# Kernel optimization log

Measured on AMD Instinct MI355X. Metric: run time of the kernel, lower is better.

Reference implementation:

```python
import jax, jax.numpy as jnp
import numpy as np

B, C, H, W = 16, 256, 32, 32
DIM = H * W  # LayerNorm/Linear dim == h*w per the rearrange in forward


def _conv1x1(x, w, b):
    # x: [b,c,h,w], w: [out,in] (1x1 kernel squeezed), b: [out]
    return jnp.einsum('bchw,oc->bohw', x, w) + b[None, :, None, None]


def _layernorm(x, g, b, eps=1e-5):
    mu = jnp.mean(x, axis=-1, keepdims=True)
    var = jnp.var(x, axis=-1, keepdims=True)
    return (x - mu) / jnp.sqrt(var + eps) * g + b


def setup_inputs() -> dict:
    key = jax.random.key(0)
    ks = jax.random.split(key, 12)
    n = jax.random.normal
    k_cdc = (2.0 / (2 * C)) ** 0.5   # kaiming_normal fan_in = 2C
    k_v = (2.0 / C) ** 0.5           # fan_in = C
    k_lin = (2.0 / DIM) ** 0.5       # fan_in = DIM
    return {
        'x_spa': n(ks[0], (B, C, H, W), jnp.float32),
        'x_freq': n(ks[1], (B, C, H, W), jnp.float32),
        'w_cdc': n(ks[2], (C, 2 * C), jnp.float32) * k_cdc,
        'b_cdc': jnp.zeros((C,), jnp.float32),
        'w_sv': n(ks[3], (C, C), jnp.float32) * k_v,
        'b_sv': jnp.zeros((C,), jnp.float32),
        'w_fv': n(ks[4], (C, C), jnp.float32) * k_v,
        'b_fv': jnp.zeros((C,), jnp.float32),
        'ln_w': jnp.ones((DIM,), jnp.float32),
        'ln_b': jnp.zeros((DIM,), jnp.float32),
        'w_qk': n(ks[5], (2 * DIM, DIM), jnp.float32) * k_lin,  # Linear(dim, 2*dim), no bias
        'w_spa': n(ks[6], (DIM, DIM), jnp.float32) * k_lin,
        'b_spa': jnp.zeros((DIM,), jnp.float32),
        'w_frq': n(ks[7], (DIM, DIM), jnp.float32) * k_lin,
        'b_frq': jnp.zeros((DIM,), jnp.float32),
    }


def reference(x_spa, x_freq, w_cdc, b_cdc, w_sv, b_sv, w_fv, b_fv,
              ln_w, ln_b, w_qk, w_spa, b_spa, w_frq, b_frq):
    b, c, h, w = x_spa.shape
    hw = h * w
    scale = hw ** (-0.5)
    v_spa = _conv1x1(x_spa, w_sv, b_sv).reshape(b, c, hw)
    v_freq = _conv1x1(x_freq, w_fv, b_fv).reshape(b, c, hw)
    x = _conv1x1(jnp.concatenate([x_spa, x_freq], axis=1), w_cdc, b_cdc).reshape(b, c, hw)
    x = _layernorm(x, ln_w, ln_b)
    qk = x @ w_qk.T                       # [b, c, 2*hw]
    q, k = jnp.split(qk, 2, axis=-1)      # each [b, c, hw]
    att = jnp.einsum('bcn,bcm->bnm', q, k) * scale   # q^T k over channels: [b, hw, hw]
    att_spa = jax.nn.softmax(att @ w_spa.T + b_spa, axis=-1)
    att_frq = jax.nn.softmax(att @ w_frq.T + b_frq, axis=-1)
    out_spa = x_spa + jnp.einsum('bcn,bnm->bcm', v_spa, att_spa).reshape(b, c, h, w)
    out_freq = x_freq + jnp.einsum('bcn,bnm->bcm', v_freq, att_frq).reshape(b, c, h, w)
    return out_spa, out_freq
```

## Files before the change

kernel.cpp:

```cpp
#include <hip/hip_runtime.h>
#include <hip/hip_bf16.h>

typedef __hip_bfloat16 bf16;
typedef __attribute__((ext_vector_type(8))) short bf16x8v;
typedef __attribute__((ext_vector_type(4))) float f32x4v;

__device__ __forceinline__ float bfbits2f(unsigned short h) {
    union { unsigned int u; float f; } v; v.u = ((unsigned int)h) << 16; return v.f;
}
__device__ __forceinline__ unsigned short f2bfbits(float f) {
    bf16 h = __float2bfloat16(f);
    unsigned short s;
    __builtin_memcpy(&s, &h, 2);
    return s;
}
__device__ __forceinline__ float load1_any(const void* p, long idx, bool f32) {
    if (f32) return ((const float*)p)[idx];
    return bfbits2f(((const unsigned short*)p)[idx]);
}
__device__ __forceinline__ float4 loadbf4(const bf16* p) {
    ushort4 u = *reinterpret_cast<const ushort4*>(p);
    return make_float4(bfbits2f(u.x), bfbits2f(u.y), bfbits2f(u.z), bfbits2f(u.w));
}
__device__ __forceinline__ void store_bf4(bf16* p, float a, float b, float c, float d) {
    ushort4 o;
    o.x = f2bfbits(a); o.y = f2bfbits(b); o.z = f2bfbits(c); o.w = f2bfbits(d);
    *reinterpret_cast<ushort4*>(p) = o;
}
__device__ __forceinline__ void gl16(const void* g, void* l) {
    __builtin_amdgcn_global_load_lds(
        (const __attribute__((address_space(1))) unsigned int*)g,
        (__attribute__((address_space(3))) unsigned int*)l, 16, 0, 0);
}

__global__ __launch_bounds__(1024)
void detect_kernel(const unsigned short* __restrict__ x, int* __restrict__ flag) {
    const int tid = threadIdx.x;
    int zc = 0, hc = 0;
    const uint4* xv = (const uint4*)x;
#pragma unroll
    for (int p = 0; p < 16; ++p) {
        uint4 v = xv[p * 1024 + tid];
        unsigned s0 = v.x & 0xFFFFu, s1 = v.y & 0xFFFFu;
        unsigned s2 = v.z & 0xFFFFu, s3 = v.w & 0xFFFFu;
        zc += (int)(s0 == 0) + (int)(s1 == 0) + (int)(s2 == 0) + (int)(s3 == 0);
        hc += (int)(((s0 >> 7) & 0xFFu) >= 0x90u) + (int)(((s1 >> 7) & 0xFFu) >= 0x90u)
            + (int)(((s2 >> 7) & 0xFFu) >= 0x90u) + (int)(((s3 >> 7) & 0xFFu) >= 0x90u);
    }
#pragma unroll
    for (int off = 32; off > 0; off >>= 1) {
        zc += __shfl_down(zc, off);
        hc += __shfl_down(hc, off);
    }
    __shared__ int rz[16], rh[16];
    if ((tid & 63) == 0) { rz[tid >> 6] = zc; rh[tid >> 6] = hc; }
    __syncthreads();
    if (tid == 0) {
        int Z = 0, H = 0;
#pragma unroll
        for (int i = 0; i < 16; ++i) { Z += rz[i]; H += rh[i]; }
        flag[0] = (Z > 60000 || H > 256) ? 1 : 0;
        flag[1] = 1;
    }
}

__global__ void diag_kernel(float* __restrict__ out, float val) {
    if (threadIdx.x == 0) out[0] = val;
}

__global__ __launch_bounds__(256)
void convert6_kernel(const void* __restrict__ s0, const void* __restrict__ s1,
                     const void* __restrict__ s2, const void* __restrict__ s3,
                     const void* __restrict__ s4, const void* __restrict__ s5,
                     const void* __restrict__ b0, const void* __restrict__ b1,
                     const void* __restrict__ b2,
                     bf16* __restrict__ dst, bf16* __restrict__ wl,
                     float* __restrict__ bc, const int* __restrict__ dflag) {
    const bool f32 = (*dflag != 0);
    for (long i = (long)blockIdx.x * 256 + threadIdx.x; i < 4850432;
         i += (long)gridDim.x * 256) {
        if (i < 4456448) {
            const void* s; long o;
            if (i < 131072)       { s = s0; o = i; }
            else if (i < 196608)  { s = s1; o = i - 131072; }
            else if (i < 262144)  { s = s2; o = i - 196608; }
            else if (i < 2359296) { s = s3; o = i - 262144; }
            else if (i < 3407872) { s = s4; o = i - 2359296; }
            else                  { s = s5; o = i - 3407872; }
            dst[i] = __float2bfloat16(load1_any(s, o, f32));
        } else if (i < 4849664) {
            long j = i - 4456448;
            int r = (int)(j >> 9), c = (int)(j & 511);
            float v = 0.f;
            if (r < 256) v = load1_any(s0, r * 512 + c, f32);
            else if (r < 512) { if (c < 256) v = load1_any(s1, (r - 256) * 256 + c, f32); }
            else              { if (c >= 256) v = load1_any(s2, (r - 512) * 256 + (c - 256), f32); }
            wl[j] = __float2bfloat16(v);
        } else {
            long j = i - 4849664;
            float v = (j < 256) ? load1_any(b0, j, f32)
                    : (j < 512) ? load1_any(b1, j - 256, f32)
                                : load1_any(b2, j - 512, f32);
            bc[j] = v;
        }
    }
}

__global__ __launch_bounds__(256)
void xpose_w_kernel(const bf16* __restrict__ src, bf16* __restrict__ dst) {
    __shared__ float t[64][65];
    const int c0 = blockIdx.x * 64, r0 = blockIdx.y * 64;
    const int tid = threadIdx.x;
#pragma unroll
    for (int p = 0; p < 16; ++p) {
        int e = tid + p * 256; int r = e >> 6, c = e & 63;
        t[r][c] = __bfloat162float(src[(long)(r0 + r) * 1024 + c0 + c]);
    }
    __syncthreads();
#pragma unroll
    for (int p = 0; p < 16; ++p) {
        int e = tid + p * 256; int r = e >> 6, c = e & 63;
        dst[(long)(c0 + r) * 1024 + r0 + c] = __float2bfloat16(t[c][r]);
    }
}

__global__ __launch_bounds__(256)
void xpose_conv_kernel(const void* __restrict__ x1, const void* __restrict__ x2,
                       bf16* __restrict__ dst, int bofs, int zsplit,
                       const int* __restrict__ dflag) {
    const bool f32 = (*dflag != 0);
    __shared__ float t[64][65];
    const int ch0 = blockIdx.y * 64, n0 = blockIdx.x * 64, z = blockIdx.z;
    const bool hiz = (z >= zsplit);
    const int zl = hiz ? z - zsplit : z;
    const void* x = hiz ? x2 : x1;
    const long sb = (long)(zl + bofs) * 262144, db = (long)z * 262144;
    const int tid = threadIdx.x;
#pragma unroll
    for (int p = 0; p < 16; ++p) {
        int e = tid + p * 256; int sch = e >> 6, sn = e & 63;
        t[sch][sn] = load1_any(x, sb + (long)(ch0 + sch) * 1024 + n0 + sn, f32);
    }
    __syncthreads();
#pragma unroll
    for (int p = 0; p < 16; ++p) {
        int e = tid + p * 256; int dn = e >> 6, dch = e & 63;
        dst[db + (long)(n0 + dn) * 256 + ch0 + dch] = __float2bfloat16(t[dch][dn]);
    }
}

__global__ __launch_bounds__(256)
void smnorm_kernel(bf16* __restrict__ X, bf16* __restrict__ vb, int gN, int gq) {
    const int tid = threadIdx.x;
    const int cg = tid & 7;
    const int js = tid >> 3;
    const int n0 = blockIdx.x * 64;
    const long zb = (long)blockIdx.y * 1048576;
    unsigned short* Xp = (unsigned short*)X + zb + n0 + cg * 8;

    float m[8];
#pragma unroll
    for (int q = 0; q < 8; ++q) m[q] = -3.4e38f;
#pragma unroll 4
    for (int r = 0; r < 32; ++r) {
        bf16x8v u = *(const bf16x8v*)(Xp + (long)(js * 32 + r) * 1024);
#pragma unroll
        for (int q = 0; q < 8; ++q)
            m[q] = fmaxf(m[q], bfbits2f((unsigned short)u[q]));
    }
    __shared__ float sh[32][8][8];
    __shared__ float Mc[64];
    __shared__ float Sc[64];
#pragma unroll
    for (int q = 0; q < 8; ++q) sh[js][cg][q] = m[q];
    __syncthreads();
    if (tid < 64) {
        float mm = -3.4e38f;
#pragma unroll 8
        for (int s = 0; s < 32; ++s) mm = fmaxf(mm, sh[s][tid >> 3][tid & 7]);
        Mc[tid] = mm;
    }
    __syncthreads();
    float M8[8], s8[8];
#pragma unroll
    for (int q = 0; q < 8; ++q) { M8[q] = Mc[cg * 8 + q]; s8[q] = 0.f; }
#pragma unroll 4
    for (int r = 0; r < 32; ++r) {
        long off = (long)(js * 32 + r) * 1024;
        bf16x8v u = *(const bf16x8v*)(Xp + off);
        bf16x8v o;
#pragma unroll
        for (int q = 0; q < 8; ++q) {
            float e = __expf(bfbits2f((unsigned short)u[q]) - M8[q]);
            s8[q] += e;
            o[q] = (short)f2bfbits(e);
        }
        *(bf16x8v*)(Xp + off) = o;
    }
    __syncthreads();
#pragma unroll
    for (int q = 0; q < 8; ++q) sh[js][cg][q] = s8[q];
    __syncthreads();
    if (tid < 64) {
        float ss = 0.f;
#pragma unroll 8
        for (int s = 0; s < 32; ++s) ss += sh[s][tid >> 3][tid & 7];
        Sc[tid] = 1.0f / ss;
    }
    __syncthreads();
    const int side = (blockIdx.y >= (unsigned)gq) ? 1 : 0;
    const int zl = blockIdx.y - side * gq;
    bf16* vp = vb + (long)(side * 256) * gN + (long)zl * 1024 + n0 + cg * 8;
    float is8[8];
#pragma unroll
    for (int q = 0; q < 8; ++q) is8[q] = Sc[cg * 8 + q];
#pragma unroll
    for (int rr = 0; rr < 8; ++rr) {
        long off = (long)(rr * 32 + js) * gN;
        bf16x8v u = *(bf16x8v*)(vp + off);
        bf16x8v o;
#pragma unroll
        for (int q = 0; q < 8; ++q)
            o[q] = (short)f2bfbits(bfbits2f((unsigned short)u[q]) * is8[q]);
        *(bf16x8v*)(vp + off) = o;
    }
}

template <int MI, int EPI, int NBUF>
__global__ __launch_bounds__(256)
void mfma_nt(const bf16* __restrict__ A1, const bf16* __restrict__ A2,
             long aB1, long aB2, int ldA1, int ldA2,
             const bf16* __restrict__ B1, const bf16* __restrict__ B2,
             long bB1, long bB2, int ldB1, int ldB2,
             int ksplit, long kOff2,
             void* __restrict__ out1, void* __restrict__ out2,
             long oB1, long oB2, int ldO1, int ldO2,
             int K, float scale,
             const void* __restrict__ bias1, const void* __restrict__ bias2,
             const void* __restrict__ res1, const void* __restrict__ res2,
             long rBatch, int bofs, int zsplit,
             const int* __restrict__ dflag) {
    constexpr int BM = MI * 32;
    constexpr int LPS = MI / 2 + 2;
    __shared__ short As[NBUF][BM * 32];
    __shared__ short Bs[NBUF][4096];
    const int tid  = threadIdx.x;
    const int lane = tid & 63, wave = tid >> 6;
    const int quad = lane >> 4, lrow = lane & 15;
    const int wm = (wave >> 1) * (MI * 16), wn = (wave & 1) * 64;

    int bx = blockIdx.x, by = blockIdx.y, bz = blockIdx.z;
    {
        const int gx = gridDim.x, gy = gridDim.y;
        const int gxy = gx * gy;
        const int ntot = gxy * gridDim.z;
        if ((ntot & 7) == 0) {
            int flat = bx + gx * (by + gy * bz);
            int w = (flat & 7) * (ntot >> 3) + (flat >> 3);
            bz = w / gxy;
            int rem = w - bz * gxy;
            by = rem / gx;
            bx = rem - by * gx;
        }
    }
    const int z  = bz;
    const bool hiz = (z >= zsplit);
    const int zl = hiz ? z - zsplit : z;
    const int n0 = bx * 128, m0 = by * BM;
    const int ldA = hiz ? ldA2 : ldA1, ldB = hiz ? ldB2 : ldB1;
    const int ldO = hiz ? ldO2 : ldO1;
    const int srow = tid >> 2, sseg = tid & 3;
    const int sl = sseg ^ ((srow >> 1) & 3);
    const int xq = quad ^ ((lrow >> 1) & 3);

    const bf16* Ab = (hiz ? A2 : A1) + (long)zl * (hiz ? aB2 : aB1);
    const bf16* Bb = (hiz ? B2 : B1) + (long)zl * (hiz ? bB2 : bB1);

    auto stage = [&](int buf, int k0) {
        const bf16* asrc = Ab + (long)k0;
        const bf16* bsrc = Bb + ((k0 < ksplit) ? (long)k0 : (long)(k0 - ksplit) + kOff2);
#pragma unroll
        for (int p = 0; p < MI / 2; ++p)
            gl16(asrc + (long)(m0 + p * 64 + srow) * ldA + sl * 8,
                 &As[buf][p * 2048 + wave * 512]);
        gl16(bsrc + (long)(n0 + srow) * ldB + sl * 8, &Bs[buf][wave * 512]);
        gl16(bsrc + (long)(n0 + 64 + srow) * ldB + sl * 8, &Bs[buf][2048 + wave * 512]);
    };

    f32x4v acc[MI][4] = {};
    const int nt = K >> 5;
    stage(0, 0);
    if (nt > 1) stage(1, 32);
    if constexpr (NBUF >= 5) {
        if (nt > 2) stage(2, 64);
        if (nt > 3) stage(3, 96);
    }

    int cur = 0;
    for (int t = 0; t < nt; ++t) {
        const int rem = nt - 1 - t;
        if constexpr (NBUF == 3) {
            if (rem >= 1) {
                if constexpr (LPS == 4) asm volatile("s_waitcnt vmcnt(4)" ::: "memory");
                else                    asm volatile("s_waitcnt vmcnt(3)" ::: "memory");
            } else {
                asm volatile("s_waitcnt vmcnt(0)" ::: "memory");
            }
        } else {
            if constexpr (LPS == 4) {
                if (rem >= 3)      asm volatile("s_waitcnt vmcnt(12)" ::: "memory");
                else if (rem == 2) asm volatile("s_waitcnt vmcnt(8)" ::: "memory");
                else if (rem == 1) asm volatile("s_waitcnt vmcnt(4)" ::: "memory");
                else               asm volatile("s_waitcnt vmcnt(0)" ::: "memory");
            } else {
                if (rem >= 3)      asm volatile("s_waitcnt vmcnt(9)" ::: "memory");
                else if (rem == 2) asm volatile("s_waitcnt vmcnt(6)" ::: "memory");
                else if (rem == 1) asm volatile("s_waitcnt vmcnt(3)" ::: "memory");
                else               asm volatile("s_waitcnt vmcnt(0)" ::: "memory");
            }
        }
        __builtin_amdgcn_s_barrier();
        __builtin_amdgcn_sched_barrier(0);
        if (t + NBUF - 1 < nt) {
            int nb = cur + NBUF - 1; if (nb >= NBUF) nb -= NBUF;
            stage(nb, (t + NBUF - 1) << 5);
        }
        bf16x8v bfr[4], afr[MI];
#pragma unroll
        for (int j = 0; j < 4; ++j)
            bfr[j] = *(const bf16x8v*)&Bs[cur][(wn + j * 16 + lrow) * 32 + xq * 8];
#pragma unroll
        for (int i = 0; i < MI; ++i)
            afr[i] = *(const bf16x8v*)&As[cur][(wm + i * 16 + lrow) * 32 + xq * 8];
#pragma unroll
        for (int i = 0; i < MI; ++i)
#pragma unroll
            for (int j = 0; j < 4; ++j)
                acc[i][j] = __builtin_amdgcn_mfma_f32_16x16x32_bf16(afr[i], bfr[j], acc[i][j], 0, 0, 0);
        cur = (cur + 1 == NBUF) ? 0 : cur + 1;
    }

    const bool f32 = (*dflag != 0);
    const void* bias = hiz ? bias2 : bias1;
    if (EPI != 3) {
        bf16* O = (bf16*)(hiz ? out2 : out1) + (long)zl * (hiz ? oB2 : oB1);
#pragma unroll
        for (int i = 0; i < MI; ++i) {
            int row0 = m0 + wm + i * 16 + quad * 4;
            float rb[4] = {0.f, 0.f, 0.f, 0.f};
            if (EPI == 1 || EPI == 2) {
#pragma unroll
                for (int r = 0; r < 4; ++r) rb[r] = load1_any(bias, row0 + r, f32);
            }
#pragma unroll
            for (int j = 0; j < 4; ++j) {
                int col = n0 + wn + j * 16 + lrow;
#pragma unroll
                for (int r = 0; r < 4; ++r) {
                    float vv = acc[i][j][r];
                    if (EPI == 1) vv += rb[r];
                    if (EPI == 2) vv = vv * scale + rb[r];
                    O[(long)(row0 + r) * ldO + col] = __float2bfloat16(vv);
                }
            }
        }
    } else {
        float* O = (float*)(hiz ? out2 : out1);
        const void* res = hiz ? res2 : res1;
        const long ob  = (long)(zl + bofs) * (hiz ? oB2 : oB1);
        const long rbb = (long)(zl + bofs) * rBatch;
#pragma unroll
        for (int i = 0; i < MI; ++i) {
            int row0 = m0 + wm + i * 16 + quad * 4;
#pragma unroll
            for (int j = 0; j < 4; ++j) {
                int col = n0 + wn + j * 16 + lrow;
#pragma unroll
                for (int r = 0; r < 4; ++r) {
                    float rv = load1_any(res, rbb + (long)(row0 + r) * ldO + col, f32);
                    O[ob + (long)(row0 + r) * ldO + col] = acc[i][j][r] + rv;
                }
            }
        }
    }
}

__global__ __launch_bounds__(256)
void layernorm_kernel(const bf16* __restrict__ src, bf16* __restrict__ dst,
                      const void* __restrict__ g, const void* __restrict__ beta,
                      int gN, const int* __restrict__ dflag) {
    const bool f32 = (*dflag != 0);
    const int zc = blockIdx.x;
    const int zz = zc >> 8, c = zc & 255;
    const bf16* p = src + (long)c * gN + (long)zz * 1024;
    bf16* q = dst + (long)zc * 1024;
    const int tid = threadIdx.x;
    float4 v = loadbf4(p + tid * 4);
    float s  = v.x + v.y + v.z + v.w;
    float ss = v.x * v.x + v.y * v.y + v.z * v.z + v.w * v.w;
#pragma unroll
    for (int off = 32; off > 0; off >>= 1) {
        s  += __shfl_down(s, off);
        ss += __shfl_down(ss, off);
    }
    __shared__ float sh[8];
    __shared__ float sh_mu, sh_rs;
    if ((tid & 63) == 0) { sh[tid >> 6] = s; sh[4 + (tid >> 6)] = ss; }
    __syncthreads();
    if (tid == 0) {
        float S  = sh[0] + sh[1] + sh[2] + sh[3];
        float SS = sh[4] + sh[5] + sh[6] + sh[7];
        float mu = S * (1.0f / 1024.0f);
        float var = SS * (1.0f / 1024.0f) - mu * mu;
        sh_mu = mu;
        sh_rs = rsqrtf(fmaxf(var, 0.0f) + 1e-5f);
    }
    __syncthreads();
    float mu = sh_mu, rs = sh_rs;
    float gx = load1_any(g, tid * 4 + 0, f32), gy = load1_any(g, tid * 4 + 1, f32);
    float gz = load1_any(g, tid * 4 + 2, f32), gw = load1_any(g, tid * 4 + 3, f32);
    float bx = load1_any(beta, tid * 4 + 0, f32), by = load1_any(beta, tid * 4 + 1, f32);
    float bz = load1_any(beta, tid * 4 + 2, f32), bw = load1_any(beta, tid * 4 + 3, f32);
    store_bf4(q + tid * 4,
              (v.x - mu) * rs * gx + bx, (v.y - mu) * rs * gy + by,
              (v.z - mu) * rs * gz + bz, (v.w - mu) * rs * gw + bw);
}

extern "C" void kernel_launch(void* const* d_in, const int* in_sizes, int n_in,
                              void* d_out, int out_size, void* d_ws, size_t ws_size,
                              hipStream_t stream) {
    const void* x_spa  = d_in[0];
    const void* x_freq = d_in[1];
    const void* w_cdc  = d_in[2];
    const void* b_cdc  = d_in[3];
    const void* w_sv   = d_in[4];
    const void* b_sv   = d_in[5];
    const void* w_fv   = d_in[6];
    const void* b_fv   = d_in[7];
    const void* ln_w   = d_in[8];
    const void* ln_b   = d_in[9];
    const void* w_qk   = d_in[10];
    const void* w_spa  = d_in[11];
    const void* b_spa  = d_in[12];
    const void* w_frq  = d_in[13];
    const void* b_frq  = d_in[14];
    float* out = (float*)d_out;

    const int B = 16, C = 256;
    const long XB = 262144;
    const long PB = 1048576;

    int*   dflag = (int*)d_ws;
    float* bcat  = (float*)((char*)d_ws + 1024);
    bf16*  wb    = (bf16*)((char*)d_ws + 4096);
    bf16* w_cdc_b = wb;
    bf16* w_sv_b  = w_cdc_b + 131072;
    bf16* w_fv_b  = w_sv_b  + 65536;
    bf16* w_qk_b  = w_fv_b  + 65536;
    bf16* w_spa_b = w_qk_b  + 2097152;
    bf16* w_frq_b = w_spa_b + 1048576;
    bf16* w_qk_hiT= w_frq_b + 1048576;
    bf16* W1f     = w_qk_hiT + 1048576;
    bf16* Wleft   = W1f + 1048576;
    bf16* pb      = Wleft + 393216;

    const size_t fixedB = 4096 + 6946816ull * 2;
    const size_t perB   = 8921088ull;
    size_t avail = (ws_size > fixedB) ? (ws_size - fixedB) : 0;
    long gmax = (long)(avail / perB);
    const bool wsOK = (gmax >= 1);
    int G = wsOK ? (int)(gmax > 16 ? 16 : gmax) : 1;

    bf16* xT    = pb;
    bf16* XV    = xT  + 2L * G * XB;
    bf16* xln2  = XV  + 3L * G * XB;
    bf16* qTT   = xln2 + (long)G * XB;
    bf16* attpT = qTT + 3L * G * XB;

    dim3 blk(256);
    detect_kernel<<<dim3(1), dim3(1024), 0, stream>>>((const unsigned short*)x_spa, dflag);

    if (!wsOK) {
        float mb = (float)(ws_size >> 20);
        diag_kernel<<<dim3(1), dim3(64), 0, stream>>>(out, 1000.0f * (mb + 1.0f));
        return;
    }

    convert6_kernel<<<dim3(4352), blk, 0, stream>>>(
        w_cdc, w_sv, w_fv, w_qk, w_spa, w_frq, b_cdc, b_sv, b_fv,
        wb, Wleft, bcat, dflag);
    xpose_w_kernel<<<dim3(16, 16), blk, 0, stream>>>(w_qk_b + 1048576, w_qk_hiT);
    mfma_nt<4, 0, 5><<<dim3(8, 8, 2), blk, 0, stream>>>(
        w_spa_b, w_frq_b, 0, 0, 1024, 1024,
        w_qk_hiT, w_qk_hiT, 0, 0, 1024, 1024, 1024, 0,
        w_qk_b + 1048576, W1f, 0, 0, 1024, 1024,
        1024, 1.0f, nullptr, nullptr, nullptr, nullptr, 0, 0, 1, dflag);

    for (int b0 = 0; b0 < B; b0 += G) {
        int g = (B - b0 < G) ? (B - b0) : G;
        const int gN = g * 1024;
        bf16* vb = XV + 256L * gN;

        xpose_conv_kernel<<<dim3(16, 4, 2 * g), blk, 0, stream>>>(
            x_spa, x_freq, xT, b0, g, dflag);

        mfma_nt<4, 1, 5><<<dim3(8 * g, 6, 1), blk, 0, stream>>>(
            Wleft, Wleft, 0, 0, 512, 512,
            xT, xT, 0, 0, 256, 256, 256, (long)g * XB,
            XV, XV, 0, 0, gN, gN,
            512, 1.0f, bcat, bcat, nullptr, nullptr, 0, 0, 1, dflag + 1);

        layernorm_kernel<<<dim3(g * C), blk, 0, stream>>>(XV, xln2, ln_w, ln_b, gN, dflag);

        mfma_nt<4, 0, 5><<<dim3(2 * g, 8, 3), blk, 0, stream>>>(
            w_qk_b, W1f, 1048576, 0, 1024, 1024,
            xln2, xln2, 0, 0, 1024, 1024, 1024, 0,
            qTT, qTT + 2L * g * XB, (long)g * XB, 0, g * 256, g * 256,
            1024, 1.0f, nullptr, nullptr, nullptr, nullptr, 0, 0, 2, dflag);

        mfma_nt<4, 2, 3><<<dim3(8, 8, 2 * g), blk, 0, stream>>>(
            qTT + (long)g * XB, qTT + 2L * g * XB, 256, 256, g * 256, g * 256,
            qTT, qTT, 256, 256, g * 256, g * 256, 256, 0,
            attpT, attpT + (long)g * PB, PB, PB, 1024, 1024,
            256, 0.03125f, b_spa, b_frq, nullptr, nullptr, 0, 0, g, dflag);

        smnorm_kernel<<<dim3(16, 2 * g), blk, 0, stream>>>(attpT, vb, gN, g);

        mfma_nt<4, 3, 5><<<dim3(8, 2, 2 * g), blk, 0, stream>>>(
            vb, vb + 256L * gN, 1024, 1024, gN, gN,
            attpT, attpT + (long)g * PB, PB, PB, 1024, 1024, 1024, 0,
            out, out + 4194304, XB, XB, 1024, 1024,
            1024, 1.0f, nullptr, nullptr, x_spa, x_freq, XB, b0, g, dflag);
    }
}
```

Baseline: 368.4 us.

## Fuse softmax column-max into attention GEMM epilogue via atomicMax

The attention-logit GEMM epilogue now reduces per-column maxima across waves and publishes them with an order-preserving unsigned atomicMax into a colmax buffer. The transpose kernel initialises that buffer and gains a float4 path for fp32 input. The softmax-normalise kernel reads the precomputed maxima instead of doing its own full max pass over the logits. The GEMM pipeline also drops to a fixed triple buffer with s_setprio around the MFMA block. This removes one full read of the attention matrix at the cost of atomics, an extra barrier in the epilogue, and shallower prefetch for the other GEMMs.

```diff
diff --git a/kernel.cpp b/kernel.cpp
--- a/kernel.cpp
+++ b/kernel.cpp
@@ -32,6 +32,7 @@
         (const __attribute__((address_space(1))) unsigned int*)g,
         (__attribute__((address_space(3))) unsigned int*)l, 16, 0, 0);
 }
+#define CMAX_INIT 0x00800000u
 
 __global__ __launch_bounds__(1024)
 void detect_kernel(const unsigned short* __restrict__ x, int* __restrict__ flag) {
@@ -126,8 +127,8 @@
 
 __global__ __launch_bounds__(256)
 void xpose_conv_kernel(const void* __restrict__ x1, const void* __restrict__ x2,
-                       bf16* __restrict__ dst, int bofs, int zsplit,
-                       const int* __restrict__ dflag) {
+                       bf16* __restrict__ dst, unsigned* __restrict__ colmax,
+                       int bofs, int zsplit, const int* __restrict__ dflag) {
     const bool f32 = (*dflag != 0);
     __shared__ float t[64][65];
     const int ch0 = blockIdx.y * 64, n0 = blockIdx.x * 64, z = blockIdx.z;
@@ -136,10 +137,25 @@
     const void* x = hiz ? x2 : x1;
     const long sb = (long)(zl + bofs) * 262144, db = (long)z * 262144;
     const int tid = threadIdx.x;
-#pragma unroll
-    for (int p = 0; p < 16; ++p) {
-        int e = tid + p * 256; int sch = e >> 6, sn = e & 63;
-        t[sch][sn] = load1_any(x, sb + (long)(ch0 + sch) * 1024 + n0 + sn, f32);
+    if (blockIdx.x == 0 && blockIdx.y == 0) {
+        uint4* ci = (uint4*)(colmax + (long)z * 1024) + tid;
+        *ci = make_uint4(CMAX_INIT, CMAX_INIT, CMAX_INIT, CMAX_INIT);
+    }
+    if (f32) {
+        const float* xf = (const float*)x;
+#pragma unroll
+        for (int p = 0; p < 4; ++p) {
+            int e = tid + p * 256; int sch = e >> 4, sn = (e & 15) * 4;
+            float4 v = *(const float4*)(xf + sb + (long)(ch0 + sch) * 1024 + n0 + sn);
+            t[sch][sn] = v.x; t[sch][sn + 1] = v.y;
+            t[sch][sn + 2] = v.z; t[sch][sn + 3] = v.w;
+        }
+    } else {
+#pragma unroll
+        for (int p = 0; p < 16; ++p) {
+            int e = tid + p * 256; int sch = e >> 6, sn = e & 63;
+            t[sch][sn] = bfbits2f(((const unsigned short*)x)[sb + (long)(ch0 + sch) * 1024 + n0 + sn]);
+        }
     }
     __syncthreads();
 #pragma unroll
@@ -150,40 +166,24 @@
 }
 
 __global__ __launch_bounds__(256)
-void smnorm_kernel(bf16* __restrict__ X, bf16* __restrict__ vb, int gN, int gq) {
+void smnorm_kernel(bf16* __restrict__ X, bf16* __restrict__ vb,
+                   const unsigned* __restrict__ colmax, int gN, int gq) {
     const int tid = threadIdx.x;
     const int cg = tid & 7;
     const int js = tid >> 3;
     const int n0 = blockIdx.x * 64;
     const long zb = (long)blockIdx.y * 1048576;
     unsigned short* Xp = (unsigned short*)X + zb + n0 + cg * 8;
-
-    float m[8];
-#pragma unroll
-    for (int q = 0; q < 8; ++q) m[q] = -3.4e38f;
-#pragma unroll 4
-    for (int r = 0; r < 32; ++r) {
-        bf16x8v u = *(const bf16x8v*)(Xp + (long)(js * 32 + r) * 1024);
-#pragma unroll
-        for (int q = 0; q < 8; ++q)
-            m[q] = fmaxf(m[q], bfbits2f((unsigned short)u[q]));
-    }
-    __shared__ float sh[32][8][8];
-    __shared__ float Mc[64];
-    __shared__ float Sc[64];
-#pragma unroll
-    for (int q = 0; q < 8; ++q) sh[js][cg][q] = m[q];
-    __syncthreads();
-    if (tid < 64) {
-        float mm = -3.4e38f;
-#pragma unroll 8
-        for (int s = 0; s < 32; ++s) mm = fmaxf(mm, sh[s][tid >> 3][tid & 7]);
-        Mc[tid] = mm;
-    }
-    __syncthreads();
+    const unsigned* cm = colmax + (long)blockIdx.y * 1024 + n0 + cg * 8;
+
     float M8[8], s8[8];
 #pragma unroll
-    for (int q = 0; q < 8; ++q) { M8[q] = Mc[cg * 8 + q]; s8[q] = 0.f; }
+    for (int q = 0; q < 8; ++q) {
+        unsigned k = cm[q];
+        unsigned b = (k & 0x80000000u) ? (k & 0x7fffffffu) : ~k;
+        M8[q] = __uint_as_float(b);
+        s8[q] = 0.f;
+    }
 #pragma unroll 4
     for (int r = 0; r < 32; ++r) {
         long off = (long)(js * 32 + r) * 1024;
@@ -197,7 +197,8 @@
         }
         *(bf16x8v*)(Xp + off) = o;
     }
-    __syncthreads();
+    __shared__ float sh[32][8][8];
+    __shared__ float Sc[64];
 #pragma unroll
     for (int q = 0; q < 8; ++q) sh[js][cg][q] = s8[q];
     __syncthreads();
@@ -226,7 +227,7 @@
     }
 }
 
-template <int MI, int EPI, int NBUF>
+template <int MI, int EPI>
 __global__ __launch_bounds__(256)
 void mfma_nt(const bf16* __restrict__ A1, const bf16* __restrict__ A2,
              long aB1, long aB2, int ldA1, int ldA2,
@@ -241,9 +242,8 @@
              long rBatch, int bofs, int zsplit,
              const int* __restrict__ dflag) {
     constexpr int BM = MI * 32;
-    constexpr int LPS = MI / 2 + 2;
-    __shared__ short As[NBUF][BM * 32];
-    __shared__ short Bs[NBUF][4096];
+    __shared__ short As[3][BM * 32];
+    __shared__ short Bs[3][4096];
     const int tid  = threadIdx.x;
     const int lane = tid & 63, wave = tid >> 6;
     const int quad = lane >> 4, lrow = lane & 15;
@@ -291,39 +291,20 @@
     const int nt = K >> 5;
     stage(0, 0);
     if (nt > 1) stage(1, 32);
-    if constexpr (NBUF >= 5) {
-        if (nt > 2) stage(2, 64);
-        if (nt > 3) stage(3, 96);
-    }
 
     int cur = 0;
     for (int t = 0; t < nt; ++t) {
-        const int rem = nt - 1 - t;
-        if constexpr (NBUF == 3) {
-            if (rem >= 1) {
-                if constexpr (LPS == 4) asm volatile("s_waitcnt vmcnt(4)" ::: "memory");
-                else                    asm volatile("s_waitcnt vmcnt(3)" ::: "memory");
-            } else {
-                asm volatile("s_waitcnt vmcnt(0)" ::: "memory");
-            }
+        if (t + 1 < nt) {
+            if constexpr (MI == 4) asm volatile("s_waitcnt vmcnt(4)" ::: "memory");
+            else                   asm volatile("s_waitcnt vmcnt(3)" ::: "memory");
         } else {
-            if constexpr (LPS == 4) {
-                if (rem >= 3)      asm volatile("s_waitcnt vmcnt(12)" ::: "memory");
-                else if (rem == 2) asm volatile("s_waitcnt vmcnt(8)" ::: "memory");
-                else if (rem == 1) asm volatile("s_waitcnt vmcnt(4)" ::: "memory");
-                else               asm volatile("s_waitcnt vmcnt(0)" ::: "memory");
-            } else {
-                if (rem >= 3)      asm volatile("s_waitcnt vmcnt(9)" ::: "memory");
-                else if (rem == 2) asm volatile("s_waitcnt vmcnt(6)" ::: "memory");
-                else if (rem == 1) asm volatile("s_waitcnt vmcnt(3)" ::: "memory");
-                else               asm volatile("s_waitcnt vmcnt(0)" ::: "memory");
-            }
+            asm volatile("s_waitcnt vmcnt(0)" ::: "memory");
         }
         __builtin_amdgcn_s_barrier();
         __builtin_amdgcn_sched_barrier(0);
-        if (t + NBUF - 1 < nt) {
-            int nb = cur + NBUF - 1; if (nb >= NBUF) nb -= NBUF;
-            stage(nb, (t + NBUF - 1) << 5);
+        if (t + 2 < nt) {
+            int nb = cur + 2; if (nb >= 3) nb -= 3;
+            stage(nb, (t + 2) << 5);
         }
         bf16x8v bfr[4], afr[MI];
 #pragma unroll
@@ -332,18 +313,21 @@
 #pragma unroll
         for (int i = 0; i < MI; ++i)
             afr[i] = *(const bf16x8v*)&As[cur][(wm + i * 16 + lrow) * 32 + xq * 8];
+        __builtin_amdgcn_s_setprio(1);
 #pragma unroll
         for (int i = 0; i < MI; ++i)
 #pragma unroll
             for (int j = 0; j < 4; ++j)
                 acc[i][j] = __builtin_amdgcn_mfma_f32_16x16x32_bf16(afr[i], bfr[j], acc[i][j], 0, 0, 0);
-        cur = (cur + 1 == NBUF) ? 0 : cur + 1;
+        __builtin_amdgcn_s_setprio(0);
+        cur = (cur == 2) ? 0 : cur + 1;
     }
 
     const bool f32 = (*dflag != 0);
     const void* bias = hiz ? bias2 : bias1;
     if (EPI != 3) {
         bf16* O = (bf16*)(hiz ? out2 : out1) + (long)zl * (hiz ? oB2 : oB1);
+        float colm[4] = {-3.4e38f, -3.4e38f, -3.4e38f, -3.4e38f};
 #pragma unroll
         for (int i = 0; i < MI; ++i) {
             int row0 = m0 + wm + i * 16 + quad * 4;
@@ -359,9 +343,30 @@
                 for (int r = 0; r < 4; ++r) {
                     float vv = acc[i][j][r];
                     if (EPI == 1) vv += rb[r];
-                    if (EPI == 2) vv = vv * scale + rb[r];
+                    if (EPI == 2) { vv = vv * scale + rb[r]; colm[j] = fmaxf(colm[j], vv); }
                     O[(long)(row0 + r) * ldO + col] = __float2bfloat16(vv);
                 }
+            }
+        }
+        if constexpr (EPI == 2) {
+            __shared__ float smx[2][128];
+#pragma unroll
+            for (int off = 16; off < 64; off <<= 1)
+#pragma unroll
+                for (int j = 0; j < 4; ++j)
+                    colm[j] = fmaxf(colm[j], __shfl_xor(colm[j], off));
+            if (quad == 0) {
+#pragma unroll
+                for (int j = 0; j < 4; ++j)
+                    smx[wave >> 1][wn + j * 16 + lrow] = colm[j];
+            }
+            __syncthreads();
+            if (tid < 128) {
+                float M = fmaxf(smx[0][tid], smx[1][tid]);
+                unsigned b = __float_as_uint(M);
+                unsigned key = (b & 0x80000000u) ? ~b : (b | 0x80000000u);
+                unsigned* cmp = (unsigned*)(hiz ? res2 : res1) + (long)zl * rBatch + n0 + tid;
+                atomicMax(cmp, key);
             }
         }
     } else {
@@ -476,6 +481,7 @@
     bf16* xln2  = XV  + 3L * G * XB;
     bf16* qTT   = xln2 + (long)G * XB;
     bf16* attpT = qTT + 3L * G * XB;
+    unsigned* colmax = (unsigned*)(attpT + 2L * G * PB);
 
     dim3 blk(256);
     detect_kernel<<<dim3(1), dim3(1024), 0, stream>>>((const unsigned short*)x_spa, dflag);
@@ -490,7 +496,7 @@
         w_cdc, w_sv, w_fv, w_qk, w_spa, w_frq, b_cdc, b_sv, b_fv,
         wb, Wleft, bcat, dflag);
     xpose_w_kernel<<<dim3(16, 16), blk, 0, stream>>>(w_qk_b + 1048576, w_qk_hiT);
-    mfma_nt<4, 0, 5><<<dim3(8, 8, 2), blk, 0, stream>>>(
+    mfma_nt<4, 0><<<dim3(8, 8, 2), blk, 0, stream>>>(
         w_spa_b, w_frq_b, 0, 0, 1024, 1024,
         w_qk_hiT, w_qk_hiT, 0, 0, 1024, 1024, 1024, 0,
         w_qk_b + 1048576, W1f, 0, 0, 1024, 1024,
@@ -502,9 +508,9 @@
         bf16* vb = XV + 256L * gN;
 
         xpose_conv_kernel<<<dim3(16, 4, 2 * g), blk, 0, stream>>>(
-            x_spa, x_freq, xT, b0, g, dflag);
-
-        mfma_nt<4, 1, 5><<<dim3(8 * g, 6, 1), blk, 0, stream>>>(
+            x_spa, x_freq, xT, colmax, b0, g, dflag);
+
+        mfma_nt<4, 1><<<dim3(8 * g, 6, 1), blk, 0, stream>>>(
             Wleft, Wleft, 0, 0, 512, 512,
             xT, xT, 0, 0, 256, 256, 256, (long)g * XB,
             XV, XV, 0, 0, gN, gN,
@@ -512,21 +518,22 @@
 
         layernorm_kernel<<<dim3(g * C), blk, 0, stream>>>(XV, xln2, ln_w, ln_b, gN, dflag);
 
-        mfma_nt<4, 0, 5><<<dim3(2 * g, 8, 3), blk, 0, stream>>>(
+        mfma_nt<4, 0><<<dim3(2 * g, 8, 3), blk, 0, stream>>>(
             w_qk_b, W1f, 1048576, 0, 1024, 1024,
             xln2, xln2, 0, 0, 1024, 1024, 1024, 0,
             qTT, qTT + 2L * g * XB, (long)g * XB, 0, g * 256, g * 256,
             1024, 1.0f, nullptr, nullptr, nullptr, nullptr, 0, 0, 2, dflag);
 
-        mfma_nt<4, 2, 3><<<dim3(8, 8, 2 * g), blk, 0, stream>>>(
+        mfma_nt<4, 2><<<dim3(8, 8, 2 * g), blk, 0, stream>>>(
             qTT + (long)g * XB, qTT + 2L * g * XB, 256, 256, g * 256, g * 256,
             qTT, qTT, 256, 256, g * 256, g * 256, 256, 0,
             attpT, attpT + (long)g * PB, PB, PB, 1024, 1024,
-            256, 0.03125f, b_spa, b_frq, nullptr, nullptr, 0, 0, g, dflag);
-
-        smnorm_kernel<<<dim3(16, 2 * g), blk, 0, stream>>>(attpT, vb, gN, g);
-
-        mfma_nt<4, 3, 5><<<dim3(8, 2, 2 * g), blk, 0, stream>>>(
+            256, 0.03125f, b_spa, b_frq, colmax, colmax + (long)g * 1024,
+            1024, 0, g, dflag);
+
+        smnorm_kernel<<<dim3(16, 2 * g), blk, 0, stream>>>(attpT, vb, colmax, gN, g);
+
+        mfma_nt<4, 3><<<dim3(8, 2, 2 * g), blk, 0, stream>>>(
             vb, vb + 256L * gN, 1024, 1024, gN, gN,
             attpT, attpT + (long)g * PB, PB, PB, 1024, 1024, 1024, 0,
             out, out + 4194304, XB, XB, 1024, 1024,
```

Result: faster. 336.9 us (-8.6%).
